# Optimization experiments

Hardware: AMD Instinct MI355X
Metric: run time of the kernel (lower is better)

The kernel has to match this reference:

```python
import jax, jax.numpy as jnp
import numpy as np

QD, KD, HID, NH = 256, 320, 256, 8
NQ, NK, NB = 4096, 4096, 16
DH = HID // NH
EPS = 1e-5
SCALE = float(1.0 / np.sqrt(DH))


def setup_inputs() -> dict:
    key = jax.random.key(0)
    ks = jax.random.split(key, 12)
    s = 0.02
    return {
        "query_nodes": jax.random.normal(ks[0], (NQ, QD), jnp.float32),
        "key_nodes": jax.random.normal(ks[1], (NK, KD), jnp.float32),
        "Wq": jax.random.normal(ks[2], (QD, HID), jnp.float32) * s,
        "bq": jnp.zeros((HID,), jnp.float32),
        "Wk": jax.random.normal(ks[3], (KD, HID), jnp.float32) * s,
        "bk": jnp.zeros((HID,), jnp.float32),
        "Wv": jax.random.normal(ks[4], (KD, HID), jnp.float32) * s,
        "bv": jnp.zeros((HID,), jnp.float32),
        "in_proj_w": jax.random.normal(ks[5], (3 * HID, HID), jnp.float32) * s,
        "in_proj_b": jnp.zeros((3 * HID,), jnp.float32),
        "mha_ow": jax.random.normal(ks[6], (HID, HID), jnp.float32) * s,
        "mha_ob": jnp.zeros((HID,), jnp.float32),
        "Wo": jax.random.normal(ks[7], (HID, QD), jnp.float32) * s,
        "bo": jnp.zeros((QD,), jnp.float32),
        "ln_g": jnp.ones((QD,), jnp.float32),
        "ln_b": jnp.zeros((QD,), jnp.float32),
        "query_batch_idx": jnp.sort(jax.random.randint(ks[8], (NQ,), 0, NB, jnp.int32)),
        "key_batch_idx": jnp.sort(jax.random.randint(ks[9], (NK,), 0, NB, jnp.int32)),
    }


def reference(query_nodes, key_nodes, Wq, bq, Wk, bk, Wv, bv, in_proj_w, in_proj_b,
              mha_ow, mha_ob, Wo, bo, ln_g, ln_b, query_batch_idx, key_batch_idx):
    # outer projections
    q = query_nodes @ Wq + bq          # [NQ, HID]
    k = key_nodes @ Wk + bk            # [NK, HID]
    v = key_nodes @ Wv + bv            # [NK, HID]
    # nn.MultiheadAttention internal in_proj (weights stored [3H, H], applied as x @ W.T)
    q2 = q @ in_proj_w[:HID].T + in_proj_b[:HID]
    k2 = k @ in_proj_w[HID:2 * HID].T + in_proj_b[HID:2 * HID]
    v2 = v @ in_proj_w[2 * HID:].T + in_proj_b[2 * HID:]
    qh = q2.reshape(NQ, NH, DH)
    kh = k2.reshape(NK, NH, DH)
    vh = v2.reshape(NK, NH, DH)
    scores = jnp.einsum('qhd,khd->hqk', qh, kh) * SCALE   # [NH, NQ, NK]
    mask = query_batch_idx[:, None] != key_batch_idx[None, :]  # True = disallowed
    scores = jnp.where(mask[None], -jnp.inf, scores)
    attn = jax.nn.softmax(scores, axis=-1)
    ctx = jnp.einsum('hqk,khd->qhd', attn, vh).reshape(NQ, HID)
    ctx = ctx @ mha_ow + mha_ob        # MHA internal out_proj
    out = ctx @ Wo + bo                # module out_proj back to query_dim
    x = query_nodes + out              # residual (dropout is identity in eval)
    mu = jnp.mean(x, axis=-1, keepdims=True)
    var = jnp.mean((x - mu) ** 2, axis=-1, keepdims=True)
    return (x - mu) / jnp.sqrt(var + EPS) * ln_g + ln_b
```

## Files before the change

### kernel.cpp

```cpp
#include <hip/hip_runtime.h>
#include <hip/hip_bf16.h>
#include <math.h>

#define NQ 4096
#define NK 4096
#define QD 256
#define KD 320
#define HID 256
#define NH 8
#define DH 32
#define NB 16
#define LN_EPS 1e-5f
#define ATT_SCALE 0.17677669529663687f

typedef unsigned short ushort_t;
typedef __attribute__((ext_vector_type(8))) short bf16x8_t;
typedef __attribute__((ext_vector_type(4))) short bf16x4_t;
typedef __attribute__((ext_vector_type(4))) float f32x4_t;

#define OFF_Q2B   0
#define OFF_K2B   524288
#define OFF_V2B   1048576
#define OFF_CTXB  1572864
#define OFF_WQT   2097152
#define OFF_WKT   2129920
#define OFF_WVT   2170880
#define OFF_WOT   2211840
#define OFF_BEFF  2244608
#define OFF_KST   2245632
#define OFF_KEN   2245648
#define OFF_FLAG  2245664

struct KArgs {
    const void* in[18];
    float* ws;
    void* out;
};

__device__ __forceinline__ float bf16_bits_to_f(ushort_t s) {
    unsigned int u = (unsigned int)s << 16;
    float f;
    __builtin_memcpy(&f, &u, 4);
    return f;
}

__device__ __forceinline__ ushort_t f_to_bf16_bits(float v) {
    __hip_bfloat16 t = (__hip_bfloat16)v;
    ushort_t b;
    __builtin_memcpy(&b, &t, 2);
    return b;
}

template <bool F32>
__device__ __forceinline__ bf16x8_t ld8(const void* p, size_t idx) {
    if constexpr (!F32) {
        return *(const bf16x8_t*)((const ushort_t*)p + idx);
    } else {
        f32x4_t f0 = *(const f32x4_t*)((const float*)p + idx);
        f32x4_t f1 = *(const f32x4_t*)((const float*)p + idx + 4);
        bf16x8_t h;
#pragma unroll
        for (int e = 0; e < 4; ++e) h[e] = (short)f_to_bf16_bits(f0[e]);
#pragma unroll
        for (int e = 0; e < 4; ++e) h[4 + e] = (short)f_to_bf16_bits(f1[e]);
        return h;
    }
}

template <bool F32>
__device__ __forceinline__ float ld1f(const void* p, size_t idx) {
    if constexpr (F32) return ((const float*)p)[idx];
    else               return bf16_bits_to_f(((const ushort_t*)p)[idx]);
}

template <bool F32>
__device__ __forceinline__ ushort_t ld1h(const void* p, size_t idx) {
    if constexpr (F32) return f_to_bf16_bits(((const float*)p)[idx]);
    else               return ((const ushort_t*)p)[idx];
}

__device__ __forceinline__ int detect_flag(const void* probe_v, int tid) {
    __shared__ float s_red[4];
    const ushort_t* probe = (const ushort_t*)probe_v;
    float mx = 0.f;
    for (int i = tid; i < 4096; i += 256) {
        float f = fabsf(bf16_bits_to_f(probe[i]));
        if (!(f == f)) f = 1e38f;
        mx = fmaxf(mx, f);
    }
    for (int off = 32; off; off >>= 1) mx = fmaxf(mx, __shfl_xor(mx, off, 64));
    if ((tid & 63) == 0) s_red[tid >> 6] = mx;
    __syncthreads();
    float m2 = fmaxf(fmaxf(s_red[0], s_red[1]), fmaxf(s_red[2], s_red[3]));
    return (m2 < 100.f) ? 1 : 0;
}

template <bool F32>
__device__ __forceinline__ void fuse_qkv_tile(const void* A, size_t abase,
                                              const void* B, ushort_t* Out,
                                              int N, int m0, int n0,
                                              int col, int quad) {
    f32x4_t acc[4];
#pragma unroll
    for (int t = 0; t < 4; ++t) acc[t] = (f32x4_t){0.f, 0.f, 0.f, 0.f};
    size_t aoff = abase + (size_t)(m0 + col) * 256 + quad * 8;
    size_t boff = (size_t)(n0 + col) * 256 + quad * 8;
#pragma unroll
    for (int kc = 0; kc < 256; kc += 32) {
        bf16x8_t af = ld8<F32>(A, aoff + kc);
#pragma unroll
        for (int t = 0; t < 4; ++t) {
            bf16x8_t bf = ld8<F32>(B, boff + (size_t)t * 16 * 256 + kc);
            acc[t] = __builtin_amdgcn_mfma_f32_16x16x32_bf16(af, bf, acc[t], 0, 0, 0);
        }
    }
#pragma unroll
    for (int t = 0; t < 4; ++t)
#pragma unroll
        for (int rr = 0; rr < 4; ++rr)
            Out[(size_t)(m0 + quad * 4 + rr) * N + n0 + t * 16 + col] =
                f_to_bf16_bits(acc[t][rr]);
}

template <bool F32>
__device__ __forceinline__ void fuse_o_tile(const void* Wo, const void* Mow,
                                            ushort_t* Out, int m0, int n0,
                                            int col, int quad) {
    f32x4_t acc[4];
#pragma unroll
    for (int t = 0; t < 4; ++t) acc[t] = (f32x4_t){0.f, 0.f, 0.f, 0.f};
#pragma unroll
    for (int kc = 0; kc < 256; kc += 32) {
        bf16x8_t af;
#pragma unroll
        for (int t = 0; t < 8; ++t)
            af[t] = (short)ld1h<F32>(Wo, (size_t)(kc + quad * 8 + t) * 256 + m0 + col);
#pragma unroll
        for (int t = 0; t < 4; ++t) {
            bf16x8_t bf = ld8<F32>(Mow, (size_t)(n0 + t * 16 + col) * 256 + quad * 8 + kc);
            acc[t] = __builtin_amdgcn_mfma_f32_16x16x32_bf16(af, bf, acc[t], 0, 0, 0);
        }
    }
#pragma unroll
    for (int t = 0; t < 4; ++t)
#pragma unroll
        for (int rr = 0; rr < 4; ++rr)
            Out[(size_t)(m0 + quad * 4 + rr) * 256 + n0 + t * 16 + col] =
                f_to_bf16_bits(acc[t][rr]);
}

template <bool F32>
__device__ __forceinline__ void bias_body(KArgs& a, float* ws, int m, int tid) {
    __shared__ float bsh[256];
    float* beff = ws + OFF_BEFF;
    if (m < 3) {
        const void* bsrc = (m == 0) ? a.in[3] : (m == 1) ? a.in[5] : a.in[7];
        bsh[tid] = ld1f<F32>(bsrc, tid);
        __syncthreads();
        float acc = 0.f;
        size_t row = (size_t)(m * 256 + tid) * 256;
#pragma unroll 4
        for (int kc = 0; kc < 256; kc += 8) {
            bf16x8_t wr = ld8<F32>(a.in[8], row + kc);
#pragma unroll
            for (int t = 0; t < 8; ++t)
                acc += bsh[kc + t] * bf16_bits_to_f((ushort_t)wr[t]);
        }
        acc += ld1f<F32>(a.in[9], m * 256 + tid);
        beff[m * 256 + tid] = acc;
    } else {
        bsh[tid] = ld1f<F32>(a.in[11], tid);
        __syncthreads();
        float acc = 0.f;
        for (int k = 0; k < 256; ++k)
            acc += bsh[k] * ld1f<F32>(a.in[12], (size_t)k * 256 + tid);
        acc += ld1f<F32>(a.in[13], tid);
        beff[3 * 256 + tid] = acc;
    }
}

__global__ __launch_bounds__(256) void k_fuse(KArgs a) {
    float* ws = a.ws;
    const int tid = threadIdx.x, bid = blockIdx.x;
    const int lane = tid & 63, wv = tid >> 6;
    const int col = lane & 15, quad = lane >> 4;
    int fl = detect_flag(a.in[0], tid);
    if (bid == 0 && tid == 0) *(int*)(ws + OFF_FLAG) = fl;

    if (bid < 16) {
        const int* kb = (const int*)a.in[17];
        int* kstart = (int*)(ws + OFF_KST);
        int* kend   = (int*)(ws + OFF_KEN);
        int j = bid * 256 + tid;
        if (j < NK) {
            int b = kb[j];
            if (j == 0) {
                for (int x = 0; x < b; ++x) { kstart[x] = 0; kend[x] = 0; }
                kstart[b] = 0;
            } else {
                int bp = kb[j - 1];
                if (bp != b) {
                    kend[bp] = j;
                    for (int x = bp + 1; x < b; ++x) { kstart[x] = j; kend[x] = j; }
                    kstart[b] = j;
                }
            }
            if (j == NK - 1) {
                kend[b] = NK;
                for (int x = b + 1; x < NB; ++x) { kstart[x] = NK; kend[x] = NK; }
            }
        }
    } else if (bid < 88) {
        int r = bid - 16;
        const void* A; const void* B; ushort_t* Out;
        size_t abase; int N, mb, nb, typ;
        if (r < 16)      { typ = 0; A = a.in[8]; abase = 0;      B = a.in[2]; Out = (ushort_t*)(ws + OFF_WQT); N = 256; mb = r >> 2; nb = r & 3; }
        else if (r < 36) { typ = 0; int rr = r - 16; A = a.in[8]; abase = 65536;  B = a.in[4]; Out = (ushort_t*)(ws + OFF_WKT); N = 320; mb = rr / 5; nb = rr % 5; }
        else if (r < 56) { typ = 0; int rr = r - 36; A = a.in[8]; abase = 131072; B = a.in[6]; Out = (ushort_t*)(ws + OFF_WVT); N = 320; mb = rr / 5; nb = rr % 5; }
        else             { typ = 1; int rr = r - 56; A = a.in[12]; abase = 0; B = a.in[10]; Out = (ushort_t*)(ws + OFF_WOT); N = 256; mb = rr >> 2; nb = rr & 3; }
        int m0 = mb * 64 + wv * 16, n0 = nb * 64;
        if (typ == 0) {
            if (fl) fuse_qkv_tile<false>(A, abase, B, Out, N, m0, n0, col, quad);
            else    fuse_qkv_tile<true >(A, abase, B, Out, N, m0, n0, col, quad);
        } else {
            if (fl) fuse_o_tile<false>(A, B, Out, m0, n0, col, quad);
            else    fuse_o_tile<true >(A, B, Out, m0, n0, col, quad);
        }
    } else {
        int m = bid - 88;
        if (fl) bias_body<false>(a, ws, m, tid);
        else    bias_body<true >(a, ws, m, tid);
    }
}

template <bool F32, int KK>
__device__ __forceinline__ void proj_body(const void* X, const ushort_t* WT,
                                          const float* bias, ushort_t* Z,
                                          int m0, int n0, int col, int quad) {
    f32x4_t acc[4];
#pragma unroll
    for (int t = 0; t < 4; ++t) acc[t] = (f32x4_t){0.f, 0.f, 0.f, 0.f};
    size_t aoff = (size_t)(m0 + col) * KK + quad * 8;
    const ushort_t* Wrow = WT + (size_t)(n0 + col) * KK + quad * 8;
#pragma unroll
    for (int kc = 0; kc < KK; kc += 32) {
        bf16x8_t af = ld8<F32>(X, aoff + kc);
#pragma unroll
        for (int t = 0; t < 4; ++t) {
            bf16x8_t bf = *(const bf16x8_t*)(Wrow + (size_t)t * 16 * KK + kc);
            acc[t] = __builtin_amdgcn_mfma_f32_16x16x32_bf16(af, bf, acc[t], 0, 0, 0);
        }
    }
#pragma unroll
    for (int t = 0; t < 4; ++t)
#pragma unroll
        for (int rr = 0; rr < 4; ++rr) {
            int n = n0 + t * 16 + col;
            Z[(size_t)(m0 + quad * 4 + rr) * 256 + n] =
                f_to_bf16_bits(acc[t][rr] + bias[n]);
        }
}

__global__ __launch_bounds__(256) void k_qkv(KArgs a) {
    float* ws = a.ws;
    const int tid = threadIdx.x, u = blockIdx.x;
    const int lane = tid & 63, wv = tid >> 6;
    const int col = lane & 15, quad = lane >> 4;
    const int fl = *(const int*)(ws + OFF_FLAG);
    const float* beff = ws + OFF_BEFF;

    if (u < 256) {
        int m0 = (u >> 2) * 64 + wv * 16, n0 = (u & 3) * 64;
        const ushort_t* WT = (const ushort_t*)(ws + OFF_WQT);
        ushort_t* Z = (ushort_t*)(ws + OFF_Q2B);
        if (fl) proj_body<false, 256>(a.in[0], WT, beff, Z, m0, n0, col, quad);
        else    proj_body<true , 256>(a.in[0], WT, beff, Z, m0, n0, col, quad);
    } else if (u < 512) {
        int uu = u - 256;
        int m0 = (uu >> 2) * 64 + wv * 16, n0 = (uu & 3) * 64;
        const ushort_t* WT = (const ushort_t*)(ws + OFF_WKT);
        ushort_t* Z = (ushort_t*)(ws + OFF_K2B);
        if (fl) proj_body<false, 320>(a.in[1], WT, beff + 256, Z, m0, n0, col, quad);
        else    proj_body<true , 320>(a.in[1], WT, beff + 256, Z, m0, n0, col, quad);
    } else {
        int uu = u - 512;
        int m0 = (uu >> 2) * 64 + wv * 16, n0 = (uu & 3) * 64;
        const ushort_t* WT = (const ushort_t*)(ws + OFF_WVT);
        ushort_t* Z = (ushort_t*)(ws + OFF_V2B);
        if (fl) proj_body<false, 320>(a.in[1], WT, beff + 512, Z, m0, n0, col, quad);
        else    proj_body<true , 320>(a.in[1], WT, beff + 512, Z, m0, n0, col, quad);
    }
}

__global__ __launch_bounds__(256) void k_attn(KArgs a) {
    float* ws = a.ws;
    const ushort_t* q2b = (const ushort_t*)(ws + OFF_Q2B);
    const ushort_t* k2b = (const ushort_t*)(ws + OFF_K2B);
    const ushort_t* v2b = (const ushort_t*)(ws + OFF_V2B);
    const int* qb  = (const int*)a.in[16];
    const int* kst = (const int*)(ws + OFF_KST);
    const int* ken = (const int*)(ws + OFF_KEN);
    ushort_t* ctxb = (ushort_t*)(ws + OFF_CTXB);

    int wave = threadIdx.x >> 6;
    int lane = threadIdx.x & 63;
    int qt = blockIdx.x >> 1;
    int h  = ((blockIdx.x & 1) << 2) | wave;
    int q0 = qt * 16;
    int col  = lane & 15;
    int quad = lane >> 4;

    int qq = q0 + col;
    int bq_ = qb[qq];
    int j0q = kst[bq_], j1q = ken[bq_];
    int jlo = j0q, jhi = j1q;
#pragma unroll
    for (int off = 1; off < 16; off <<= 1) {
        jlo = min(jlo, __shfl_xor(jlo, off, 64));
        jhi = max(jhi, __shfl_xor(jhi, off, 64));
    }

    bf16x8_t qf = *(const bf16x8_t*)(q2b + (size_t)qq * HID + h * DH + quad * 8);

    f32x4_t accO = {0.f, 0.f, 0.f, 0.f};
    float l_st = 0.f;

    for (int kt = jlo; kt < jhi; kt += 16) {
        int krow = kt + col;
        if (krow > NK - 1) krow = NK - 1;
        bf16x8_t kf = *(const bf16x8_t*)(k2b + (size_t)krow * HID + h * DH + quad * 8);
        ushort_t vr[4];
#pragma unroll
        for (int j = 0; j < 4; ++j) {
            int vrow = kt + quad * 4 + j;
            if (vrow > NK - 1) vrow = NK - 1;
            vr[j] = v2b[(size_t)vrow * HID + h * DH + col];
        }
        f32x4_t S = __builtin_amdgcn_mfma_f32_16x16x32_bf16(
            kf, qf, (f32x4_t){0.f, 0.f, 0.f, 0.f}, 0, 0, 0);

        bf16x4_t pb, vb;
#pragma unroll
        for (int r = 0; r < 4; ++r) {
            int kk = kt + quad * 4 + r;
            bool ok = (kk >= j0q) && (kk < j1q);
            float p = ok ? __expf(S[r] * ATT_SCALE) : 0.f;
            l_st += p;
            pb[r] = (short)f_to_bf16_bits(p);
            vb[r] = (short)vr[r];
        }
        accO = __builtin_amdgcn_mfma_f32_16x16x16bf16_1k(pb, vb, accO, 0, 0, 0);
    }

    l_st += __shfl_xor(l_st, 16, 64);
    l_st += __shfl_xor(l_st, 32, 64);

#pragma unroll
    for (int r = 0; r < 4; ++r) {
        int qrow_local = quad * 4 + r;
        float lq = __shfl(l_st, qrow_local, 64);
        float o = (lq > 0.f) ? accO[r] / lq : 0.f;
        int qrow = q0 + qrow_local;
        ctxb[(size_t)qrow * HID + h * DH + col] = f_to_bf16_bits(o);
    }
}

template <bool F32>
__device__ __forceinline__ void oln_body(KArgs& a, float* ws, int u,
                                         int wv, int col, int quad, int fl) {
    const ushort_t* ctxb = (const ushort_t*)(ws + OFF_CTXB);
    const ushort_t* wot  = (const ushort_t*)(ws + OFF_WOT);
    const float* beffO = ws + OFF_BEFF + 3 * 256;

    int m0 = u * 64 + wv * 16;
    f32x4_t acc[16];
#pragma unroll
    for (int t = 0; t < 16; ++t) acc[t] = (f32x4_t){0.f, 0.f, 0.f, 0.f};
    const ushort_t* Xrow = ctxb + (size_t)(m0 + col) * 256 + quad * 8;
    const ushort_t* Wbase = wot + (size_t)col * 256 + quad * 8;
#pragma unroll
    for (int kc = 0; kc < 256; kc += 32) {
        bf16x8_t af = *(const bf16x8_t*)(Xrow + kc);
#pragma unroll
        for (int t = 0; t < 16; ++t) {
            bf16x8_t bf = *(const bf16x8_t*)(Wbase + (size_t)t * 16 * 256 + kc);
            acc[t] = __builtin_amdgcn_mfma_f32_16x16x32_bf16(af, bf, acc[t], 0, 0, 0);
        }
    }
    float s_[4] = {0.f, 0.f, 0.f, 0.f};
    float ss_[4] = {0.f, 0.f, 0.f, 0.f};
#pragma unroll
    for (int t = 0; t < 16; ++t) {
        int n = t * 16 + col;
        float b = beffO[n];
#pragma unroll
        for (int rr = 0; rr < 4; ++rr) {
            int m = m0 + quad * 4 + rr;
            float x = acc[t][rr] + b + ld1f<F32>(a.in[0], (size_t)m * 256 + n);
            acc[t][rr] = x;
            s_[rr] += x;
            ss_[rr] += x * x;
        }
    }
#pragma unroll
    for (int off = 1; off < 16; off <<= 1) {
#pragma unroll
        for (int rr = 0; rr < 4; ++rr) {
            s_[rr]  += __shfl_xor(s_[rr],  off, 16);
            ss_[rr] += __shfl_xor(ss_[rr], off, 16);
        }
    }
    float mu[4], inv[4];
#pragma unroll
    for (int rr = 0; rr < 4; ++rr) {
        mu[rr] = s_[rr] * (1.f / QD);
        float var = ss_[rr] * (1.f / QD) - mu[rr] * mu[rr];
        inv[rr] = rsqrtf(var + LN_EPS);
    }
#pragma unroll
    for (int t = 0; t < 16; ++t) {
        int n = t * 16 + col;
        float g = ld1f<F32>(a.in[14], n), bb = ld1f<F32>(a.in[15], n);
#pragma unroll
        for (int rr = 0; rr < 4; ++rr) {
            int m = m0 + quad * 4 + rr;
            float y = (acc[t][rr] - mu[rr]) * inv[rr] * g + bb;
            size_t idx = (size_t)m * 256 + n;
            if (fl) ((ushort_t*)a.out)[idx] = f_to_bf16_bits(y);
            else    ((float*)a.out)[idx] = y;
        }
    }
}

__global__ __launch_bounds__(256) void k_oln(KArgs a) {
    float* ws = a.ws;
    const int tid = threadIdx.x;
    const int lane = tid & 63, wv = tid >> 6;
    const int col = lane & 15, quad = lane >> 4;
    const int fl = *(const int*)(ws + OFF_FLAG);
    if (fl) oln_body<false>(a, ws, blockIdx.x, wv, col, quad, fl);
    else    oln_body<true >(a, ws, blockIdx.x, wv, col, quad, fl);
}

extern "C" void kernel_launch(void* const* d_in, const int* in_sizes, int n_in,
                              void* d_out, int out_size, void* d_ws, size_t ws_size,
                              hipStream_t stream) {
    KArgs a;
    for (int i = 0; i < 18; ++i) a.in[i] = d_in[i];
    a.ws = (float*)d_ws;
    a.out = d_out;

    k_fuse<<<92, 256, 0, stream>>>(a);
    k_qkv<<<768, 256, 0, stream>>>(a);
    k_attn<<<512, 256, 0, stream>>>(a);
    k_oln<<<64, 256, 0, stream>>>(a);
}
```

Measured before the change: 162.8 us.

## Fuse four kernel launches into one cooperative megakernel with grid syncs

Merges the weight-fusion, QKV projection, attention and output/LayerNorm stages into a single cooperative kernel of 512 blocks, separated by grid-wide barriers. This removes three kernel-launch gaps and the inter-kernel drain between stages. In exchange every block waits on grid syncs, the QKV stage is spread unevenly across blocks (some do two units), and most blocks sit idle in the first and last phases. If the cooperative launch fails, it falls back to the original four launches.

Result: slower. 518.0 us (+218.3%).

```diff
diff --git a/kernel.cpp b/kernel.cpp
--- a/kernel.cpp
+++ b/kernel.cpp
@@ -1,6 +1,9 @@
 #include <hip/hip_runtime.h>
+#include <hip/hip_cooperative_groups.h>
 #include <hip/hip_bf16.h>
 #include <math.h>
+
+namespace cg = cooperative_groups;
 
 #define NQ 4096
 #define NK 4096
@@ -92,7 +95,33 @@
     if ((tid & 63) == 0) s_red[tid >> 6] = mx;
     __syncthreads();
     float m2 = fmaxf(fmaxf(s_red[0], s_red[1]), fmaxf(s_red[2], s_red[3]));
+    __syncthreads();
     return (m2 < 100.f) ? 1 : 0;
+}
+
+__device__ __forceinline__ void ranges_body(KArgs& a, float* ws, int bid, int tid) {
+    const int* kb = (const int*)a.in[17];
+    int* kstart = (int*)(ws + OFF_KST);
+    int* kend   = (int*)(ws + OFF_KEN);
+    int j = bid * 256 + tid;
+    if (j < NK) {
+        int b = kb[j];
+        if (j == 0) {
+            for (int x = 0; x < b; ++x) { kstart[x] = 0; kend[x] = 0; }
+            kstart[b] = 0;
+        } else {
+            int bp = kb[j - 1];
+            if (bp != b) {
+                kend[bp] = j;
+                for (int x = bp + 1; x < b; ++x) { kstart[x] = j; kend[x] = j; }
+                kstart[b] = j;
+            }
+        }
+        if (j == NK - 1) {
+            kend[b] = NK;
+            for (int x = b + 1; x < NB; ++x) { kstart[x] = NK; kend[x] = NK; }
+        }
+    }
 }
 
 template <bool F32>
@@ -147,6 +176,21 @@
         for (int rr = 0; rr < 4; ++rr)
             Out[(size_t)(m0 + quad * 4 + rr) * 256 + n0 + t * 16 + col] =
                 f_to_bf16_bits(acc[t][rr]);
+}
+
+template <bool F32>
+__device__ __forceinline__ void fuse_dispatch(KArgs& a, float* ws, int r,
+                                              int wv, int col, int quad, int fl) {
+    const void* A; const void* B; ushort_t* Out;
+    size_t abase; int N, mb, nb, typ;
+    if (r < 16)      { typ = 0; A = a.in[8]; abase = 0;      B = a.in[2]; Out = (ushort_t*)(ws + OFF_WQT); N = 256; mb = r >> 2; nb = r & 3; }
+    else if (r < 36) { typ = 0; int rr = r - 16; A = a.in[8]; abase = 65536;  B = a.in[4]; Out = (ushort_t*)(ws + OFF_WKT); N = 320; mb = rr / 5; nb = rr % 5; }
+    else if (r < 56) { typ = 0; int rr = r - 36; A = a.in[8]; abase = 131072; B = a.in[6]; Out = (ushort_t*)(ws + OFF_WVT); N = 320; mb = rr / 5; nb = rr % 5; }
+    else             { typ = 1; int rr = r - 56; A = a.in[12]; abase = 0; B = a.in[10]; Out = (ushort_t*)(ws + OFF_WOT); N = 256; mb = rr >> 2; nb = rr & 3; }
+    int m0 = mb * 64 + wv * 16, n0 = nb * 64;
+    if (typ == 0) fuse_qkv_tile<F32>(A, abase, B, Out, N, m0, n0, col, quad);
+    else          fuse_o_tile<F32>(A, B, Out, m0, n0, col, quad);
+    (void)fl;
 }
 
 template <bool F32>
@@ -179,6 +223,244 @@
     }
 }
 
+template <bool MEGA>
+__device__ __forceinline__ void p1_body(KArgs& a, float* ws, int bid, int tid,
+                                        int wv, int col, int quad, int fl) {
+    if (bid < 16) {
+        ranges_body(a, ws, bid, tid);
+    } else if (bid < 88) {
+        int r = bid - 16;
+        if (fl) fuse_dispatch<false>(a, ws, r, wv, col, quad, fl);
+        else    fuse_dispatch<true >(a, ws, r, wv, col, quad, fl);
+    } else if (bid < 92) {
+        int m = bid - 88;
+        if (fl) bias_body<false>(a, ws, m, tid);
+        else    bias_body<true >(a, ws, m, tid);
+    }
+}
+
+template <bool F32, int KK>
+__device__ __forceinline__ void proj_body(const void* X, const ushort_t* WT,
+                                          const float* bias, ushort_t* Z,
+                                          int m0, int n0, int col, int quad) {
+    f32x4_t acc[4];
+#pragma unroll
+    for (int t = 0; t < 4; ++t) acc[t] = (f32x4_t){0.f, 0.f, 0.f, 0.f};
+    size_t aoff = (size_t)(m0 + col) * KK + quad * 8;
+    const ushort_t* Wrow = WT + (size_t)(n0 + col) * KK + quad * 8;
+#pragma unroll
+    for (int kc = 0; kc < KK; kc += 32) {
+        bf16x8_t af = ld8<F32>(X, aoff + kc);
+#pragma unroll
+        for (int t = 0; t < 4; ++t) {
+            bf16x8_t bf = *(const bf16x8_t*)(Wrow + (size_t)t * 16 * KK + kc);
+            acc[t] = __builtin_amdgcn_mfma_f32_16x16x32_bf16(af, bf, acc[t], 0, 0, 0);
+        }
+    }
+#pragma unroll
+    for (int t = 0; t < 4; ++t)
+#pragma unroll
+        for (int rr = 0; rr < 4; ++rr) {
+            int n = n0 + t * 16 + col;
+            Z[(size_t)(m0 + quad * 4 + rr) * 256 + n] =
+                f_to_bf16_bits(acc[t][rr] + bias[n]);
+        }
+}
+
+template <bool F32>
+__device__ __forceinline__ void qkv_unit(KArgs& a, float* ws, int u,
+                                         int wv, int col, int quad) {
+    const float* beff = ws + OFF_BEFF;
+    if (u < 256) {
+        int m0 = (u >> 2) * 64 + wv * 16, n0 = (u & 3) * 64;
+        const ushort_t* WT = (const ushort_t*)(ws + OFF_WQT);
+        ushort_t* Z = (ushort_t*)(ws + OFF_Q2B);
+        proj_body<F32, 256>(a.in[0], WT, beff, Z, m0, n0, col, quad);
+    } else if (u < 512) {
+        int uu = u - 256;
+        int m0 = (uu >> 2) * 64 + wv * 16, n0 = (uu & 3) * 64;
+        const ushort_t* WT = (const ushort_t*)(ws + OFF_WKT);
+        ushort_t* Z = (ushort_t*)(ws + OFF_K2B);
+        proj_body<F32, 320>(a.in[1], WT, beff + 256, Z, m0, n0, col, quad);
+    } else {
+        int uu = u - 512;
+        int m0 = (uu >> 2) * 64 + wv * 16, n0 = (uu & 3) * 64;
+        const ushort_t* WT = (const ushort_t*)(ws + OFF_WVT);
+        ushort_t* Z = (ushort_t*)(ws + OFF_V2B);
+        proj_body<F32, 320>(a.in[1], WT, beff + 512, Z, m0, n0, col, quad);
+    }
+}
+
+__device__ __forceinline__ void attn_body(KArgs& a, float* ws, int bid,
+                                          int wv, int lane) {
+    const ushort_t* q2b = (const ushort_t*)(ws + OFF_Q2B);
+    const ushort_t* k2b = (const ushort_t*)(ws + OFF_K2B);
+    const ushort_t* v2b = (const ushort_t*)(ws + OFF_V2B);
+    const int* qb  = (const int*)a.in[16];
+    const int* kst = (const int*)(ws + OFF_KST);
+    const int* ken = (const int*)(ws + OFF_KEN);
+    ushort_t* ctxb = (ushort_t*)(ws + OFF_CTXB);
+
+    int qt = bid >> 1;
+    int h  = ((bid & 1) << 2) | wv;
+    int q0 = qt * 16;
+    int col  = lane & 15;
+    int quad = lane >> 4;
+
+    int qq = q0 + col;
+    int bq_ = qb[qq];
+    int j0q = kst[bq_], j1q = ken[bq_];
+    int jlo = j0q, jhi = j1q;
+#pragma unroll
+    for (int off = 1; off < 16; off <<= 1) {
+        jlo = min(jlo, __shfl_xor(jlo, off, 64));
+        jhi = max(jhi, __shfl_xor(jhi, off, 64));
+    }
+
+    bf16x8_t qf = *(const bf16x8_t*)(q2b + (size_t)qq * HID + h * DH + quad * 8);
+
+    f32x4_t accO = {0.f, 0.f, 0.f, 0.f};
+    float l_st = 0.f;
+
+    for (int kt = jlo; kt < jhi; kt += 16) {
+        int krow = kt + col;
+        if (krow > NK - 1) krow = NK - 1;
+        bf16x8_t kf = *(const bf16x8_t*)(k2b + (size_t)krow * HID + h * DH + quad * 8);
+        ushort_t vr[4];
+#pragma unroll
+        for (int j = 0; j < 4; ++j) {
+            int vrow = kt + quad * 4 + j;
+            if (vrow > NK - 1) vrow = NK - 1;
+            vr[j] = v2b[(size_t)vrow * HID + h * DH + col];
+        }
+        f32x4_t S = __builtin_amdgcn_mfma_f32_16x16x32_bf16(
+            kf, qf, (f32x4_t){0.f, 0.f, 0.f, 0.f}, 0, 0, 0);
+
+        bf16x4_t pb, vb;
+#pragma unroll
+        for (int r = 0; r < 4; ++r) {
+            int kk = kt + quad * 4 + r;
+            bool ok = (kk >= j0q) && (kk < j1q);
+            float p = ok ? __expf(S[r] * ATT_SCALE) : 0.f;
+            l_st += p;
+            pb[r] = (short)f_to_bf16_bits(p);
+            vb[r] = (short)vr[r];
+        }
+        accO = __builtin_amdgcn_mfma_f32_16x16x16bf16_1k(pb, vb, accO, 0, 0, 0);
+    }
+
+    l_st += __shfl_xor(l_st, 16, 64);
+    l_st += __shfl_xor(l_st, 32, 64);
+
+#pragma unroll
+    for (int r = 0; r < 4; ++r) {
+        int qrow_local = quad * 4 + r;
+        float lq = __shfl(l_st, qrow_local, 64);
+        float o = (lq > 0.f) ? accO[r] / lq : 0.f;
+        int qrow = q0 + qrow_local;
+        ctxb[(size_t)qrow * HID + h * DH + col] = f_to_bf16_bits(o);
+    }
+}
+
+template <bool F32>
+__device__ __forceinline__ void oln_body(KArgs& a, float* ws, int u,
+                                         int wv, int col, int quad, int fl) {
+    const ushort_t* ctxb = (const ushort_t*)(ws + OFF_CTXB);
+    const ushort_t* wot  = (const ushort_t*)(ws + OFF_WOT);
+    const float* beffO = ws + OFF_BEFF + 3 * 256;
+
+    int m0 = u * 64 + wv * 16;
+    f32x4_t acc[16];
+#pragma unroll
+    for (int t = 0; t < 16; ++t) acc[t] = (f32x4_t){0.f, 0.f, 0.f, 0.f};
+    const ushort_t* Xrow = ctxb + (size_t)(m0 + col) * 256 + quad * 8;
+    const ushort_t* Wbase = wot + (size_t)col * 256 + quad * 8;
+#pragma unroll
+    for (int kc = 0; kc < 256; kc += 32) {
+        bf16x8_t af = *(const bf16x8_t*)(Xrow + kc);
+#pragma unroll
+        for (int t = 0; t < 16; ++t) {
+            bf16x8_t bf = *(const bf16x8_t*)(Wbase + (size_t)t * 16 * 256 + kc);
+            acc[t] = __builtin_amdgcn_mfma_f32_16x16x32_bf16(af, bf, acc[t], 0, 0, 0);
+        }
+    }
+    float s_[4] = {0.f, 0.f, 0.f, 0.f};
+    float ss_[4] = {0.f, 0.f, 0.f, 0.f};
+#pragma unroll
+    for (int t = 0; t < 16; ++t) {
+        int n = t * 16 + col;
+        float b = beffO[n];
+#pragma unroll
+        for (int rr = 0; rr < 4; ++rr) {
+            int m = m0 + quad * 4 + rr;
+            float x = acc[t][rr] + b + ld1f<F32>(a.in[0], (size_t)m * 256 + n);
+            acc[t][rr] = x;
+            s_[rr] += x;
+            ss_[rr] += x * x;
+        }
+    }
+#pragma unroll
+    for (int off = 1; off < 16; off <<= 1) {
+#pragma unroll
+        for (int rr = 0; rr < 4; ++rr) {
+            s_[rr]  += __shfl_xor(s_[rr],  off, 16);
+            ss_[rr] += __shfl_xor(ss_[rr], off, 16);
+        }
+    }
+    float mu[4], inv[4];
+#pragma unroll
+    for (int rr = 0; rr < 4; ++rr) {
+        mu[rr] = s_[rr] * (1.f / QD);
+        float var = ss_[rr] * (1.f / QD) - mu[rr] * mu[rr];
+        inv[rr] = rsqrtf(var + LN_EPS);
+    }
+#pragma unroll
+    for (int t = 0; t < 16; ++t) {
+        int n = t * 16 + col;
+        float g = ld1f<F32>(a.in[14], n), bb = ld1f<F32>(a.in[15], n);
+#pragma unroll
+        for (int rr = 0; rr < 4; ++rr) {
+            int m = m0 + quad * 4 + rr;
+            float y = (acc[t][rr] - mu[rr]) * inv[rr] * g + bb;
+            size_t idx = (size_t)m * 256 + n;
+            if (fl) ((ushort_t*)a.out)[idx] = f_to_bf16_bits(y);
+            else    ((float*)a.out)[idx] = y;
+        }
+    }
+}
+
+__global__ __launch_bounds__(256, 2) void k_mega(KArgs a) {
+    cg::grid_group grid = cg::this_grid();
+    float* ws = a.ws;
+    const int tid = threadIdx.x, bid = blockIdx.x;
+    const int lane = tid & 63, wv = tid >> 6;
+    const int col = lane & 15, quad = lane >> 4;
+    const int fl = detect_flag(a.in[0], tid);
+
+    p1_body<true>(a, ws, bid, tid, wv, col, quad, fl);
+
+    __threadfence();
+    grid.sync();
+
+    for (int u = bid; u < 768; u += 512) {
+        if (fl) qkv_unit<false>(a, ws, u, wv, col, quad);
+        else    qkv_unit<true >(a, ws, u, wv, col, quad);
+    }
+
+    __threadfence();
+    grid.sync();
+
+    attn_body(a, ws, bid, wv, lane);
+
+    __threadfence();
+    grid.sync();
+
+    if (bid < 64) {
+        if (fl) oln_body<false>(a, ws, bid, wv, col, quad, fl);
+        else    oln_body<true >(a, ws, bid, wv, col, quad, fl);
+    }
+}
+
 __global__ __launch_bounds__(256) void k_fuse(KArgs a) {
     float* ws = a.ws;
     const int tid = threadIdx.x, bid = blockIdx.x;
@@ -186,79 +468,7 @@
     const int col = lane & 15, quad = lane >> 4;
     int fl = detect_flag(a.in[0], tid);
     if (bid == 0 && tid == 0) *(int*)(ws + OFF_FLAG) = fl;
-
-    if (bid < 16) {
-        const int* kb = (const int*)a.in[17];
-        int* kstart = (int*)(ws + OFF_KST);
-        int* kend   = (int*)(ws + OFF_KEN);
-        int j = bid * 256 + tid;
-        if (j < NK) {
-            int b = kb[j];
-            if (j == 0) {
-                for (int x = 0; x < b; ++x) { kstart[x] = 0; kend[x] = 0; }
-                kstart[b] = 0;
-            } else {
-                int bp = kb[j - 1];
-                if (bp != b) {
-                    kend[bp] = j;
-                    for (int x = bp + 1; x < b; ++x) { kstart[x] = j; kend[x] = j; }
-                    kstart[b] = j;
-                }
-            }
-            if (j == NK - 1) {
-                kend[b] = NK;
-                for (int x = b + 1; x < NB; ++x) { kstart[x] = NK; kend[x] = NK; }
-            }
-        }
-    } else if (bid < 88) {
-        int r = bid - 16;
-        const void* A; const void* B; ushort_t* Out;
-        size_t abase; int N, mb, nb, typ;
-        if (r < 16)      { typ = 0; A = a.in[8]; abase = 0;      B = a.in[2]; Out = (ushort_t*)(ws + OFF_WQT); N = 256; mb = r >> 2; nb = r & 3; }
-        else if (r < 36) { typ = 0; int rr = r - 16; A = a.in[8]; abase = 65536;  B = a.in[4]; Out = (ushort_t*)(ws + OFF_WKT); N = 320; mb = rr / 5; nb = rr % 5; }
-        else if (r < 56) { typ = 0; int rr = r - 36; A = a.in[8]; abase = 131072; B = a.in[6]; Out = (ushort_t*)(ws + OFF_WVT); N = 320; mb = rr / 5; nb = rr % 5; }
-        else             { typ = 1; int rr = r - 56; A = a.in[12]; abase = 0; B = a.in[10]; Out = (ushort_t*)(ws + OFF_WOT); N = 256; mb = rr >> 2; nb = rr & 3; }
-        int m0 = mb * 64 + wv * 16, n0 = nb * 64;
-        if (typ == 0) {
-            if (fl) fuse_qkv_tile<false>(A, abase, B, Out, N, m0, n0, col, quad);
-            else    fuse_qkv_tile<true >(A, abase, B, Out, N, m0, n0, col, quad);
-        } else {
-            if (fl) fuse_o_tile<false>(A, B, Out, m0, n0, col, quad);
-            else    fuse_o_tile<true >(A, B, Out, m0, n0, col, quad);
-        }
-    } else {
-        int m = bid - 88;
-        if (fl) bias_body<false>(a, ws, m, tid);
-        else    bias_body<true >(a, ws, m, tid);
-    }
-}
-
-template <bool F32, int KK>
-__device__ __forceinline__ void proj_body(const void* X, const ushort_t* WT,
-                                          const float* bias, ushort_t* Z,
-                                          int m0, int n0, int col, int quad) {
-    f32x4_t acc[4];
-#pragma unroll
-    for (int t = 0; t < 4; ++t) acc[t] = (f32x4_t){0.f, 0.f, 0.f, 0.f};
-    size_t aoff = (size_t)(m0 + col) * KK + quad * 8;
-    const ushort_t* Wrow = WT + (size_t)(n0 + col) * KK + quad * 8;
-#pragma unroll
-    for (int kc = 0; kc < KK; kc += 32) {
-        bf16x8_t af = ld8<F32>(X, aoff + kc);
-#pragma unroll
-        for (int t = 0; t < 4; ++t) {
-            bf16x8_t bf = *(const bf16x8_t*)(Wrow + (size_t)t * 16 * KK + kc);
-            acc[t] = __builtin_amdgcn_mfma_f32_16x16x32_bf16(af, bf, acc[t], 0, 0, 0);
-        }
-    }
-#pragma unroll
-    for (int t = 0; t < 4; ++t)
-#pragma unroll
-        for (int rr = 0; rr < 4; ++rr) {
-            int n = n0 + t * 16 + col;
-            Z[(size_t)(m0 + quad * 4 + rr) * 256 + n] =
-                f_to_bf16_bits(acc[t][rr] + bias[n]);
-        }
+    p1_body<false>(a, ws, bid, tid, wv, col, quad, fl);
 }
 
 __global__ __launch_bounds__(256) void k_qkv(KArgs a) {
@@ -267,169 +477,12 @@
     const int lane = tid & 63, wv = tid >> 6;
     const int col = lane & 15, quad = lane >> 4;
     const int fl = *(const int*)(ws + OFF_FLAG);
-    const float* beff = ws + OFF_BEFF;
-
-    if (u < 256) {
-        int m0 = (u >> 2) * 64 + wv * 16, n0 = (u & 3) * 64;
-        const ushort_t* WT = (const ushort_t*)(ws + OFF_WQT);
-        ushort_t* Z = (ushort_t*)(ws + OFF_Q2B);
-        if (fl) proj_body<false, 256>(a.in[0], WT, beff, Z, m0, n0, col, quad);
-        else    proj_body<true , 256>(a.in[0], WT, beff, Z, m0, n0, col, quad);
-    } else if (u < 512) {
-        int uu = u - 256;
-        int m0 = (uu >> 2) * 64 + wv * 16, n0 = (uu & 3) * 64;
-        const ushort_t* WT = (const ushort_t*)(ws + OFF_WKT);
-        ushort_t* Z = (ushort_t*)(ws + OFF_K2B);
-        if (fl) proj_body<false, 320>(a.in[1], WT, beff + 256, Z, m0, n0, col, quad);
-        else    proj_body<true , 320>(a.in[1], WT, beff + 256, Z, m0, n0, col, quad);
-    } else {
-        int uu = u - 512;
-        int m0 = (uu >> 2) * 64 + wv * 16, n0 = (uu & 3) * 64;
-        const ushort_t* WT = (const ushort_t*)(ws + OFF_WVT);
-        ushort_t* Z = (ushort_t*)(ws + OFF_V2B);
-        if (fl) proj_body<false, 320>(a.in[1], WT, beff + 512, Z, m0, n0, col, quad);
-        else    proj_body<true , 320>(a.in[1], WT, beff + 512, Z, m0, n0, col, quad);
-    }
+    if (fl) qkv_unit<false>(a, ws, u, wv, col, quad);
+    else    qkv_unit<true >(a, ws, u, wv, col, quad);
 }
 
 __global__ __launch_bounds__(256) void k_attn(KArgs a) {
-    float* ws = a.ws;
-    const ushort_t* q2b = (const ushort_t*)(ws + OFF_Q2B);
-    const ushort_t* k2b = (const ushort_t*)(ws + OFF_K2B);
-    const ushort_t* v2b = (const ushort_t*)(ws + OFF_V2B);
-    const int* qb  = (const int*)a.in[16];
-    const int* kst = (const int*)(ws + OFF_KST);
-    const int* ken = (const int*)(ws + OFF_KEN);
-    ushort_t* ctxb = (ushort_t*)(ws + OFF_CTXB);
-
-    int wave = threadIdx.x >> 6;
-    int lane = threadIdx.x & 63;
-    int qt = blockIdx.x >> 1;
-    int h  = ((blockIdx.x & 1) << 2) | wave;
-    int q0 = qt * 16;
-    int col  = lane & 15;
-    int quad = lane >> 4;
-
-    int qq = q0 + col;
-    int bq_ = qb[qq];
-    int j0q = kst[bq_], j1q = ken[bq_];
-    int jlo = j0q, jhi = j1q;
-#pragma unroll
-    for (int off = 1; off < 16; off <<= 1) {
-        jlo = min(jlo, __shfl_xor(jlo, off, 64));
-        jhi = max(jhi, __shfl_xor(jhi, off, 64));
-    }
-
-    bf16x8_t qf = *(const bf16x8_t*)(q2b + (size_t)qq * HID + h * DH + quad * 8);
-
-    f32x4_t accO = {0.f, 0.f, 0.f, 0.f};
-    float l_st = 0.f;
-
-    for (int kt = jlo; kt < jhi; kt += 16) {
-        int krow = kt + col;
-        if (krow > NK - 1) krow = NK - 1;
-        bf16x8_t kf = *(const bf16x8_t*)(k2b + (size_t)krow * HID + h * DH + quad * 8);
-        ushort_t vr[4];
-#pragma unroll
-        for (int j = 0; j < 4; ++j) {
-            int vrow = kt + quad * 4 + j;
-            if (vrow > NK - 1) vrow = NK - 1;
-            vr[j] = v2b[(size_t)vrow * HID + h * DH + col];
-        }
-        f32x4_t S = __builtin_amdgcn_mfma_f32_16x16x32_bf16(
-            kf, qf, (f32x4_t){0.f, 0.f, 0.f, 0.f}, 0, 0, 0);
-
-        bf16x4_t pb, vb;
-#pragma unroll
-        for (int r = 0; r < 4; ++r) {
-            int kk = kt + quad * 4 + r;
-            bool ok = (kk >= j0q) && (kk < j1q);
-            float p = ok ? __expf(S[r] * ATT_SCALE) : 0.f;
-            l_st += p;
-            pb[r] = (short)f_to_bf16_bits(p);
-            vb[r] = (short)vr[r];
-        }
-        accO = __builtin_amdgcn_mfma_f32_16x16x16bf16_1k(pb, vb, accO, 0, 0, 0);
-    }
-
-    l_st += __shfl_xor(l_st, 16, 64);
-    l_st += __shfl_xor(l_st, 32, 64);
-
-#pragma unroll
-    for (int r = 0; r < 4; ++r) {
-        int qrow_local = quad * 4 + r;
-        float lq = __shfl(l_st, qrow_local, 64);
-        float o = (lq > 0.f) ? accO[r] / lq : 0.f;
-        int qrow = q0 + qrow_local;
-        ctxb[(size_t)qrow * HID + h * DH + col] = f_to_bf16_bits(o);
-    }
-}
-
-template <bool F32>
-__device__ __forceinline__ void oln_body(KArgs& a, float* ws, int u,
-                                         int wv, int col, int quad, int fl) {
-    const ushort_t* ctxb = (const ushort_t*)(ws + OFF_CTXB);
-    const ushort_t* wot  = (const ushort_t*)(ws + OFF_WOT);
-    const float* beffO = ws + OFF_BEFF + 3 * 256;
-
-    int m0 = u * 64 + wv * 16;
-    f32x4_t acc[16];
-#pragma unroll
-    for (int t = 0; t < 16; ++t) acc[t] = (f32x4_t){0.f, 0.f, 0.f, 0.f};
-    const ushort_t* Xrow = ctxb + (size_t)(m0 + col) * 256 + quad * 8;
-    const ushort_t* Wbase = wot + (size_t)col * 256 + quad * 8;
-#pragma unroll
-    for (int kc = 0; kc < 256; kc += 32) {
-        bf16x8_t af = *(const bf16x8_t*)(Xrow + kc);
-#pragma unroll
-        for (int t = 0; t < 16; ++t) {
-            bf16x8_t bf = *(const bf16x8_t*)(Wbase + (size_t)t * 16 * 256 + kc);
-            acc[t] = __builtin_amdgcn_mfma_f32_16x16x32_bf16(af, bf, acc[t], 0, 0, 0);
-        }
-    }
-    float s_[4] = {0.f, 0.f, 0.f, 0.f};
-    float ss_[4] = {0.f, 0.f, 0.f, 0.f};
-#pragma unroll
-    for (int t = 0; t < 16; ++t) {
-        int n = t * 16 + col;
-        float b = beffO[n];
-#pragma unroll
-        for (int rr = 0; rr < 4; ++rr) {
-            int m = m0 + quad * 4 + rr;
-            float x = acc[t][rr] + b + ld1f<F32>(a.in[0], (size_t)m * 256 + n);
-            acc[t][rr] = x;
-            s_[rr] += x;
-            ss_[rr] += x * x;
-        }
-    }
-#pragma unroll
-    for (int off = 1; off < 16; off <<= 1) {
-#pragma unroll
-        for (int rr = 0; rr < 4; ++rr) {
-            s_[rr]  += __shfl_xor(s_[rr],  off, 16);
-            ss_[rr] += __shfl_xor(ss_[rr], off, 16);
-        }
-    }
-    float mu[4], inv[4];
-#pragma unroll
-    for (int rr = 0; rr < 4; ++rr) {
-        mu[rr] = s_[rr] * (1.f / QD);
-        float var = ss_[rr] * (1.f / QD) - mu[rr] * mu[rr];
-        inv[rr] = rsqrtf(var + LN_EPS);
-    }
-#pragma unroll
-    for (int t = 0; t < 16; ++t) {
-        int n = t * 16 + col;
-        float g = ld1f<F32>(a.in[14], n), bb = ld1f<F32>(a.in[15], n);
-#pragma unroll
-        for (int rr = 0; rr < 4; ++rr) {
-            int m = m0 + quad * 4 + rr;
-            float y = (acc[t][rr] - mu[rr]) * inv[rr] * g + bb;
-            size_t idx = (size_t)m * 256 + n;
-            if (fl) ((ushort_t*)a.out)[idx] = f_to_bf16_bits(y);
-            else    ((float*)a.out)[idx] = y;
-        }
-    }
+    attn_body(a, a.ws, blockIdx.x, threadIdx.x >> 6, threadIdx.x & 63);
 }
 
 __global__ __launch_bounds__(256) void k_oln(KArgs a) {
@@ -450,8 +503,13 @@
     a.ws = (float*)d_ws;
     a.out = d_out;
 
-    k_fuse<<<92, 256, 0, stream>>>(a);
-    k_qkv<<<768, 256, 0, stream>>>(a);
-    k_attn<<<512, 256, 0, stream>>>(a);
-    k_oln<<<64, 256, 0, stream>>>(a);
-}
+    void* params[] = { (void*)&a };
+    hipError_t err = hipLaunchCooperativeKernel((const void*)k_mega, dim3(512),
+                                                dim3(256), params, 0, stream);
+    if (err != hipSuccess) {
+        k_fuse<<<92, 256, 0, stream>>>(a);
+        k_qkv<<<768, 256, 0, stream>>>(a);
+        k_attn<<<512, 256, 0, stream>>>(a);
+        k_oln<<<64, 256, 0, stream>>>(a);
+    }
+}
```

## Unroll attention key loop by two and split output-LN columns across waves

Applied to the files above, without the earlier changes.

The attention inner loop now handles two 16-key tiles per iteration, with a second independent accumulator, to expose more MFMA and memory-level parallelism. The output projection plus LayerNorm kernel now gives each block 16 rows and has the four waves split the 256 output columns, combining the LayerNorm row statistics through shared memory. This quadruples the block count from 64 to 256 to fill more compute units. A barrier is also added in the flag-detection reduction so its shared buffer is not reused early. The costs are an extra __syncthreads in the LN kernel and possible wasted work on a partial final 16-key tile in attention.

Result: faster. 148.3 us (-8.9%).

```diff
diff --git a/kernel.cpp b/kernel.cpp
--- a/kernel.cpp
+++ b/kernel.cpp
@@ -92,6 +92,7 @@
     if ((tid & 63) == 0) s_red[tid >> 6] = mx;
     __syncthreads();
     float m2 = fmaxf(fmaxf(s_red[0], s_red[1]), fmaxf(s_red[2], s_red[3]));
+    __syncthreads();
     return (m2 < 100.f) ? 1 : 0;
 }
 
@@ -322,35 +323,50 @@
 
     bf16x8_t qf = *(const bf16x8_t*)(q2b + (size_t)qq * HID + h * DH + quad * 8);
 
-    f32x4_t accO = {0.f, 0.f, 0.f, 0.f};
+    f32x4_t accO  = {0.f, 0.f, 0.f, 0.f};
+    f32x4_t accO2 = {0.f, 0.f, 0.f, 0.f};
     float l_st = 0.f;
 
-    for (int kt = jlo; kt < jhi; kt += 16) {
-        int krow = kt + col;
-        if (krow > NK - 1) krow = NK - 1;
-        bf16x8_t kf = *(const bf16x8_t*)(k2b + (size_t)krow * HID + h * DH + quad * 8);
-        ushort_t vr[4];
+    for (int kt = jlo; kt < jhi; kt += 32) {
+        int ktB = kt + 16;
+        int krowA = kt + col;   if (krowA > NK - 1) krowA = NK - 1;
+        int krowB = ktB + col;  if (krowB > NK - 1) krowB = NK - 1;
+        bf16x8_t kfA = *(const bf16x8_t*)(k2b + (size_t)krowA * HID + h * DH + quad * 8);
+        bf16x8_t kfB = *(const bf16x8_t*)(k2b + (size_t)krowB * HID + h * DH + quad * 8);
+        ushort_t vrA[4], vrB[4];
 #pragma unroll
         for (int j = 0; j < 4; ++j) {
-            int vrow = kt + quad * 4 + j;
-            if (vrow > NK - 1) vrow = NK - 1;
-            vr[j] = v2b[(size_t)vrow * HID + h * DH + col];
-        }
-        f32x4_t S = __builtin_amdgcn_mfma_f32_16x16x32_bf16(
-            kf, qf, (f32x4_t){0.f, 0.f, 0.f, 0.f}, 0, 0, 0);
-
-        bf16x4_t pb, vb;
+            int vrowA = kt + quad * 4 + j;   if (vrowA > NK - 1) vrowA = NK - 1;
+            int vrowB = ktB + quad * 4 + j;  if (vrowB > NK - 1) vrowB = NK - 1;
+            vrA[j] = v2b[(size_t)vrowA * HID + h * DH + col];
+            vrB[j] = v2b[(size_t)vrowB * HID + h * DH + col];
+        }
+        f32x4_t SA = __builtin_amdgcn_mfma_f32_16x16x32_bf16(
+            kfA, qf, (f32x4_t){0.f, 0.f, 0.f, 0.f}, 0, 0, 0);
+        f32x4_t SB = __builtin_amdgcn_mfma_f32_16x16x32_bf16(
+            kfB, qf, (f32x4_t){0.f, 0.f, 0.f, 0.f}, 0, 0, 0);
+
+        bf16x4_t pbA, vbA, pbB, vbB;
 #pragma unroll
         for (int r = 0; r < 4; ++r) {
-            int kk = kt + quad * 4 + r;
-            bool ok = (kk >= j0q) && (kk < j1q);
-            float p = ok ? __expf(S[r] * ATT_SCALE) : 0.f;
-            l_st += p;
-            pb[r] = (short)f_to_bf16_bits(p);
-            vb[r] = (short)vr[r];
-        }
-        accO = __builtin_amdgcn_mfma_f32_16x16x16bf16_1k(pb, vb, accO, 0, 0, 0);
-    }
+            int kkA = kt + quad * 4 + r;
+            bool okA = (kkA >= j0q) && (kkA < j1q);
+            float pA = okA ? __expf(SA[r] * ATT_SCALE) : 0.f;
+            l_st += pA;
+            pbA[r] = (short)f_to_bf16_bits(pA);
+            vbA[r] = (short)vrA[r];
+            int kkB = ktB + quad * 4 + r;
+            bool okB = (kkB >= j0q) && (kkB < j1q);
+            float pB = okB ? __expf(SB[r] * ATT_SCALE) : 0.f;
+            l_st += pB;
+            pbB[r] = (short)f_to_bf16_bits(pB);
+            vbB[r] = (short)vrB[r];
+        }
+        accO  = __builtin_amdgcn_mfma_f32_16x16x16bf16_1k(pbA, vbA, accO,  0, 0, 0);
+        accO2 = __builtin_amdgcn_mfma_f32_16x16x16bf16_1k(pbB, vbB, accO2, 0, 0, 0);
+    }
+#pragma unroll
+    for (int r = 0; r < 4; ++r) accO[r] += accO2[r];
 
     l_st += __shfl_xor(l_st, 16, 64);
     l_st += __shfl_xor(l_st, 32, 64);
@@ -368,36 +384,38 @@
 template <bool F32>
 __device__ __forceinline__ void oln_body(KArgs& a, float* ws, int u,
                                          int wv, int col, int quad, int fl) {
+    __shared__ float sred[4][16], ssred[4][16];
     const ushort_t* ctxb = (const ushort_t*)(ws + OFF_CTXB);
     const ushort_t* wot  = (const ushort_t*)(ws + OFF_WOT);
     const float* beffO = ws + OFF_BEFF + 3 * 256;
 
-    int m0 = u * 64 + wv * 16;
-    f32x4_t acc[16];
-#pragma unroll
-    for (int t = 0; t < 16; ++t) acc[t] = (f32x4_t){0.f, 0.f, 0.f, 0.f};
+    int m0 = u * 16;
+    f32x4_t acc[4];
+#pragma unroll
+    for (int t = 0; t < 4; ++t) acc[t] = (f32x4_t){0.f, 0.f, 0.f, 0.f};
     const ushort_t* Xrow = ctxb + (size_t)(m0 + col) * 256 + quad * 8;
     const ushort_t* Wbase = wot + (size_t)col * 256 + quad * 8;
 #pragma unroll
     for (int kc = 0; kc < 256; kc += 32) {
         bf16x8_t af = *(const bf16x8_t*)(Xrow + kc);
 #pragma unroll
-        for (int t = 0; t < 16; ++t) {
+        for (int tt = 0; tt < 4; ++tt) {
+            int t = wv * 4 + tt;
             bf16x8_t bf = *(const bf16x8_t*)(Wbase + (size_t)t * 16 * 256 + kc);
-            acc[t] = __builtin_amdgcn_mfma_f32_16x16x32_bf16(af, bf, acc[t], 0, 0, 0);
+            acc[tt] = __builtin_amdgcn_mfma_f32_16x16x32_bf16(af, bf, acc[tt], 0, 0, 0);
         }
     }
     float s_[4] = {0.f, 0.f, 0.f, 0.f};
     float ss_[4] = {0.f, 0.f, 0.f, 0.f};
 #pragma unroll
-    for (int t = 0; t < 16; ++t) {
-        int n = t * 16 + col;
+    for (int tt = 0; tt < 4; ++tt) {
+        int n = (wv * 4 + tt) * 16 + col;
         float b = beffO[n];
 #pragma unroll
         for (int rr = 0; rr < 4; ++rr) {
             int m = m0 + quad * 4 + rr;
-            float x = acc[t][rr] + b + ld1f<F32>(a.in[0], (size_t)m * 256 + n);
-            acc[t][rr] = x;
+            float x = acc[tt][rr] + b + ld1f<F32>(a.in[0], (size_t)m * 256 + n);
+            acc[tt][rr] = x;
             s_[rr] += x;
             ss_[rr] += x * x;
         }
@@ -410,21 +428,32 @@
             ss_[rr] += __shfl_xor(ss_[rr], off, 16);
         }
     }
+    if (col == 0) {
+#pragma unroll
+        for (int rr = 0; rr < 4; ++rr) {
+            sred[wv][quad * 4 + rr]  = s_[rr];
+            ssred[wv][quad * 4 + rr] = ss_[rr];
+        }
+    }
+    __syncthreads();
     float mu[4], inv[4];
 #pragma unroll
     for (int rr = 0; rr < 4; ++rr) {
-        mu[rr] = s_[rr] * (1.f / QD);
-        float var = ss_[rr] * (1.f / QD) - mu[rr] * mu[rr];
+        int row = quad * 4 + rr;
+        float ts  = sred[0][row]  + sred[1][row]  + sred[2][row]  + sred[3][row];
+        float tss = ssred[0][row] + ssred[1][row] + ssred[2][row] + ssred[3][row];
+        mu[rr] = ts * (1.f / QD);
+        float var = tss * (1.f / QD) - mu[rr] * mu[rr];
         inv[rr] = rsqrtf(var + LN_EPS);
     }
 #pragma unroll
-    for (int t = 0; t < 16; ++t) {
-        int n = t * 16 + col;
+    for (int tt = 0; tt < 4; ++tt) {
+        int n = (wv * 4 + tt) * 16 + col;
         float g = ld1f<F32>(a.in[14], n), bb = ld1f<F32>(a.in[15], n);
 #pragma unroll
         for (int rr = 0; rr < 4; ++rr) {
             int m = m0 + quad * 4 + rr;
-            float y = (acc[t][rr] - mu[rr]) * inv[rr] * g + bb;
+            float y = (acc[tt][rr] - mu[rr]) * inv[rr] * g + bb;
             size_t idx = (size_t)m * 256 + n;
             if (fl) ((ushort_t*)a.out)[idx] = f_to_bf16_bits(y);
             else    ((float*)a.out)[idx] = y;
@@ -453,5 +482,5 @@
     k_fuse<<<92, 256, 0, stream>>>(a);
     k_qkv<<<768, 256, 0, stream>>>(a);
     k_attn<<<512, 256, 0, stream>>>(a);
-    k_oln<<<64, 256, 0, stream>>>(a);
-}
+    k_oln<<<256, 256, 0, stream>>>(a);
+}
```
